# Kernel tuning notes

Hardware: AMD Instinct MI355X
Metric: run time of the kernel (lower is better)

## Reference

```python
import jax, jax.numpy as jnp
import numpy as np

KH, KW = 3, 3
PAD = (1, 1, 1, 1)  # torch F.pad order: (W_left, W_right, H_top, H_bottom)
STRIDE = 1
B, CIN, COUT, H, W = 4, 32, 32, 128, 128


def setup_inputs() -> dict:
    key = jax.random.key(0)
    k1, k2, k3, k4 = jax.random.split(key, 4)
    f = jax.random.normal(k1, (B, CIN, H, W), jnp.float32)
    # orientation field components (cos/sin of a random angle field)
    theta = jax.random.uniform(k2, (B, CIN, H, W), jnp.float32, 0.0, 2.0 * np.pi)
    r0 = jnp.cos(theta)
    r1 = jnp.sin(theta)
    # learned conv weight (nn.Conv2d default uniform init, no bias)
    fan_in = CIN * KH * KW
    bound = 1.0 / np.sqrt(fan_in)
    w = jax.random.uniform(k3, (COUT, CIN, KH, KW), jnp.float32, -bound, bound)
    # frozen wr: (randn * pi * 100) / a with a = 100  ->  randn * pi
    wr = jax.random.normal(k4, (COUT, CIN, KH, KW), jnp.float32) * np.pi
    return {"f": f, "r0": r0, "r1": r1, "w": w, "wr": wr}


def _rot90(w):
    # torch: w.permute(0,1,2,4,3).flip([4]) on the (kh,kw) dims
    return jnp.flip(jnp.swapaxes(w, -1, -2), -1)


def _conv_single(f, r0, r1, w, wr):
    # f, r0, r1: (B, Cin, Hp, Wp);  w, wr: (Cout, Cin, KH, KW)
    Hp, Wp = f.shape[2], f.shape[3]
    he = Hp - PAD[0] - PAD[1]
    we = Wp - PAD[2] - PAD[3]
    s = STRIDE
    out = None
    for i in range(KH):
        for j in range(KW):
            fw = f[:, :, i:i + he:s, j:j + we:s]    # (B, Cin, h, w)
            r0w = r0[:, :, i:i + he:s, j:j + we:s]
            r1w = r1[:, :, i:i + he:s, j:j + we:s]
            c = jnp.cos(wr[:, :, i, j])[None, :, :, None, None]   # (1, Cout, Cin, 1, 1)
            sn = jnp.sin(wr[:, :, i, j])[None, :, :, None, None]
            # lambda_theta: relu of orientation-projected field, (B, Cout, Cin, h, w)
            lam = jax.nn.relu(c * r0w[:, None] + sn * r1w[:, None])
            term = jnp.einsum('bchw,oc,bochw->bohw', fw, w[:, :, i, j], lam)
            out = term if out is None else out + term
    return out  # (B, Cout, h, w)


def _forward(f, r0, r1, w, wr):
    pl, pr, pt, pb = PAD
    pad = ((0, 0), (0, 0), (pt, pb), (pl, pr))
    fp = jnp.pad(f, pad)
    r0p = jnp.pad(r0, pad)
    r1p = jnp.pad(r1, pad)
    orient = jnp.arange(4, dtype=f.dtype) * jnp.asarray(np.pi / 2, f.dtype)
    outs = []
    wk = w
    for o in range(4):
        if o > 0:
            wk = _rot90(wk)
        outs.append(_conv_single(fp, r0p, r1p, wk, wr + orient[o]))
    stacked = jnp.stack(outs, axis=2)              # (B, Cout, 4, h, w)
    idx = jnp.argmax(stacked, axis=2)              # (B, Cout, h, w)
    out = jnp.take_along_axis(stacked, idx[:, :, None], axis=2)[:, :, 0]
    out_r = orient[idx]                            # winning orientation angle
    return out, jnp.cos(out_r), jnp.sin(out_r)


def reference(f, r0, r1, w, wr):
    return _forward(f, r0, r1, w, wr)
```

## Files before the change

kernel.cpp:

```cpp
#include <hip/hip_runtime.h>


typedef float v2f __attribute__((ext_vector_type(2)));

#define B_    4
#define CIN_  32
#define COUT_ 32
#define H_    128
#define W_    128
#define OUTSZ_ (B_ * COUT_ * H_ * W_)

#define TAB_FLOATS (CIN_ * 4 * 9 * 4 * 12)

__global__ __launch_bounds__(256)
void build_wtab(const float* __restrict__ w, const float* __restrict__ wr,
                float* __restrict__ tab)
{
    int idx = blockIdx.x * 256 + threadIdx.x;
    if (idx >= CIN_ * 4 * 9 * 4 * 2) return;
    int k    = idx & 1;
    int r    = idx >> 1;
    int pair = r & 3;
    int r2   = r >> 2;
    int tap  = r2 % 9;
    int t2   = r2 / 9;
    int ocg  = t2 & 3;
    int c    = t2 >> 2;
    int oc   = ocg * 8 + pair * 2 + k;
    int i = tap / 3, j = tap - i * 3;
    int base = (oc * CIN_ + c) * 9;
    float w0 = w[base + i * 3 + j];
    float w1 = w[base + (2 - j) * 3 + i];
    float w2 = w[base + (2 - i) * 3 + (2 - j)];
    float w3 = w[base + j * 3 + (2 - i)];
    float S, C;
    sincosf(wr[base + i * 3 + j], &S, &C);
    float* dst = tab + ((size_t)t2 * 9 + tap) * 48 + pair * 12;
    dst[0 + k]  = C;  dst[2 + k]  = S;
    dst[4 + k]  = w0; dst[6 + k]  = w1;
    dst[8 + k]  = w2; dst[10 + k] = w3;
}

__global__ __launch_bounds__(256, 4)
void orient_conv_kernel(const float* __restrict__ f,
                        const float* __restrict__ r0,
                        const float* __restrict__ r1,
                        const float* __restrict__ tab,
                        float* __restrict__ out)
{
    __shared__ float sIn[3][3][68];

    const int tid   = threadIdx.x;
    const int lane  = tid & 63;
    const int ocg   = __builtin_amdgcn_readfirstlane(tid >> 6);
    const int bid   = blockIdx.x;
    const int b     = bid >> 8;
    const int rem   = bid & 255;
    const int h     = rem >> 1;
    const int wbase = (rem & 1) << 6;

    v2f acc[4][4];
#pragma unroll
    for (int p = 0; p < 4; ++p)
#pragma unroll
        for (int o = 0; o < 4; ++o) acc[p][o] = (v2f)(0.0f);

    for (int c = 0; c < CIN_; ++c) {
        if (tid < 198) {
            int row = tid / 66;
            int col = tid - row * 66;
            int gh = h + row - 1;
            int gw = wbase + col - 1;
            bool ok = ((unsigned)gh < (unsigned)H_) & ((unsigned)gw < (unsigned)W_);
            int off = ((b * CIN_ + c) * H_ + gh) * W_ + gw;
            sIn[0][row][col] = ok ? f[off]  : 0.0f;
            sIn[1][row][col] = ok ? r0[off] : 0.0f;
            sIn[2][row][col] = ok ? r1[off] : 0.0f;
        }
        __syncthreads();

        const float* wt = tab + ((size_t)(c * 4 + ocg) * 9) * 48;

#pragma unroll
        for (int tap = 0; tap < 9; ++tap) {
            const int i = tap / 3;
            const int j = tap - i * 3;
            const int col = lane + j;
            float fv  = sIn[0][i][col];
            float r0s = sIn[1][i][col];
            float r1s = sIn[2][i][col];
            v2f fd;  fd[0]  = fv;  fd[1]  = fv;
            v2f r0d; r0d[0] = r0s; r0d[1] = r0s;
            v2f r1d; r1d[0] = r1s; r1d[1] = r1s;
            const float* wp = wt + tap * 48;
#pragma unroll
            for (int p = 0; p < 4; ++p) {
                const v2f* q = reinterpret_cast<const v2f*>(wp + p * 12);
                v2f Cv = q[0], Sv = q[1];
                v2f w0 = q[2], w1 = q[3], w2 = q[4], w3 = q[5];
                v2f u  = __builtin_elementwise_fma(Cv, r0d, Sv * r1d);
                v2f vv = __builtin_elementwise_fma(Cv, r1d, -(Sv * r0d));
                v2f g0 = __builtin_elementwise_max(u,  (v2f)(0.0f));
                v2f g1 = __builtin_elementwise_max(vv, (v2f)(0.0f));
                v2f g2 = g0 - u;
                v2f g3 = g1 - vv;
                acc[p][0] = __builtin_elementwise_fma(fd * g0, w0, acc[p][0]);
                acc[p][1] = __builtin_elementwise_fma(fd * g1, w1, acc[p][1]);
                acc[p][2] = __builtin_elementwise_fma(fd * g2, w2, acc[p][2]);
                acc[p][3] = __builtin_elementwise_fma(fd * g3, w3, acc[p][3]);
            }
        }
        __syncthreads();
    }

    const float cosv[4] = {1.0f, -4.37113883e-08f, -1.0f, 1.19248806e-08f};
    const float sinv[4] = {0.0f, 1.0f, -8.74227766e-08f, -1.0f};
    const int wcol = wbase + lane;
#pragma unroll
    for (int p = 0; p < 4; ++p) {
#pragma unroll
        for (int k = 0; k < 2; ++k) {
            int oc = ocg * 8 + p * 2 + k;
            float a0 = acc[p][0][k], a1 = acc[p][1][k];
            float a2 = acc[p][2][k], a3 = acc[p][3][k];
            float best = a0; int bi = 0;
            if (a1 > best) { best = a1; bi = 1; }
            if (a2 > best) { best = a2; bi = 2; }
            if (a3 > best) { best = a3; bi = 3; }
            size_t o = ((size_t)(b * COUT_ + oc) * H_ + h) * W_ + wcol;
            out[o]              = best;
            out[o + OUTSZ_]     = cosv[bi];
            out[o + 2 * OUTSZ_] = sinv[bi];
        }
    }
}

extern "C" void kernel_launch(void* const* d_in, const int* in_sizes, int n_in,
                              void* d_out, int out_size, void* d_ws, size_t ws_size,
                              hipStream_t stream)
{
    const float* f  = (const float*)d_in[0];
    const float* r0 = (const float*)d_in[1];
    const float* r1 = (const float*)d_in[2];
    const float* w  = (const float*)d_in[3];
    const float* wr = (const float*)d_in[4];
    float* out = (float*)d_out;
    float* tab = (float*)d_ws;

    build_wtab<<<dim3(36), dim3(256), 0, stream>>>(w, wr, tab);
    orient_conv_kernel<<<dim3(B_ * H_ * 2), dim3(256), 0, stream>>>(
        f, r0, r1, tab, out);
}
```

Measured before the change: 320.2 us.

## Remap threads to output-channel lanes with paired-pixel vectors and interleaved smem tile

Threads now map one-to-one to output channels (32 per wavefront half) and each handles 4 pixels, packed as pairs that sit 32 columns apart, where before each thread handled 8 channels for a single pixel. Blocks grow to 512 threads, and the shared tile is stored interleaved so each thread reads its neighbourhood with float4 LDS loads. The weight table is rearranged to one 8-float record per (cin, tap, oc), read per lane as a vector. The aim is to cut the work of broadcasting scalar weights and to reuse each pixel load across taps, at the cost of per-lane global weight loads and different register pressure.

```diff
diff --git a/kernel.cpp b/kernel.cpp
--- a/kernel.cpp
+++ b/kernel.cpp
@@ -10,104 +10,122 @@
 #define W_    128
 #define OUTSZ_ (B_ * COUT_ * H_ * W_)
 
-#define TAB_FLOATS (CIN_ * 4 * 9 * 4 * 12)
-
 __global__ __launch_bounds__(256)
 void build_wtab(const float* __restrict__ w, const float* __restrict__ wr,
                 float* __restrict__ tab)
 {
     int idx = blockIdx.x * 256 + threadIdx.x;
-    if (idx >= CIN_ * 4 * 9 * 4 * 2) return;
-    int k    = idx & 1;
-    int r    = idx >> 1;
-    int pair = r & 3;
-    int r2   = r >> 2;
-    int tap  = r2 % 9;
-    int t2   = r2 / 9;
-    int ocg  = t2 & 3;
-    int c    = t2 >> 2;
-    int oc   = ocg * 8 + pair * 2 + k;
+    if (idx >= CIN_ * 9 * COUT_) return;
+    int oc  = idx & 31;
+    int t2  = idx >> 5;
+    int tap = t2 % 9;
+    int cc  = t2 / 9;
     int i = tap / 3, j = tap - i * 3;
-    int base = (oc * CIN_ + c) * 9;
+    int base = (oc * CIN_ + cc) * 9;
     float w0 = w[base + i * 3 + j];
     float w1 = w[base + (2 - j) * 3 + i];
     float w2 = w[base + (2 - i) * 3 + (2 - j)];
     float w3 = w[base + j * 3 + (2 - i)];
     float S, C;
     sincosf(wr[base + i * 3 + j], &S, &C);
-    float* dst = tab + ((size_t)t2 * 9 + tap) * 48 + pair * 12;
-    dst[0 + k]  = C;  dst[2 + k]  = S;
-    dst[4 + k]  = w0; dst[6 + k]  = w1;
-    dst[8 + k]  = w2; dst[10 + k] = w3;
+    float* dst = tab + (size_t)idx * 8;
+    dst[0] = C;  dst[1] = S;
+    dst[2] = w0; dst[3] = w1;
+    dst[4] = w2; dst[5] = w3;
+    dst[6] = 0.0f; dst[7] = 0.0f;
 }
 
-__global__ __launch_bounds__(256, 4)
+__global__ __launch_bounds__(512, 4)
 void orient_conv_kernel(const float* __restrict__ f,
                         const float* __restrict__ r0,
                         const float* __restrict__ r1,
                         const float* __restrict__ tab,
                         float* __restrict__ out)
 {
-    __shared__ float sIn[3][3][68];
+    __shared__ float sF[612], sR0[612], sR1[612];
 
     const int tid   = threadIdx.x;
-    const int lane  = tid & 63;
-    const int ocg   = __builtin_amdgcn_readfirstlane(tid >> 6);
+    const int oc    = tid & 31;
+    const int pxg   = tid >> 5;
+    const int p     = pxg << 1;
     const int bid   = blockIdx.x;
     const int b     = bid >> 8;
     const int rem   = bid & 255;
     const int h     = rem >> 1;
     const int wbase = (rem & 1) << 6;
 
-    v2f acc[4][4];
+    int  r_0 = tid / 68, rm0 = tid - r_0 * 68;
+    int  c_0 = rm0 >> 1, s_0 = rm0 & 1;
+    int  gh0 = h + r_0 - 1, gw0 = wbase + c_0 + (s_0 << 5) - 1;
+    bool ok0 = ((unsigned)gh0 < (unsigned)H_) & ((unsigned)gw0 < (unsigned)W_);
+    int  go0 = ok0 ? (gh0 * W_ + gw0) : 0;
+
+    int  sl1 = tid + 512;
+    bool hv1 = sl1 < 612;
+    int  r_1 = sl1 / 68, rm1 = sl1 - r_1 * 68;
+    int  c_1 = rm1 >> 1, s_1 = rm1 & 1;
+    int  gh1 = h + r_1 - 1, gw1 = wbase + c_1 + (s_1 << 5) - 1;
+    bool ok1 = hv1 & ((unsigned)gh1 < (unsigned)H_) & ((unsigned)gw1 < (unsigned)W_);
+    int  go1 = ok1 ? (gh1 * W_ + gw1) : 0;
+
+    const int chanBase = b * (CIN_ * H_ * W_);
+
+    v2f acc[2][4];
 #pragma unroll
-    for (int p = 0; p < 4; ++p)
+    for (int q = 0; q < 2; ++q)
 #pragma unroll
-        for (int o = 0; o < 4; ++o) acc[p][o] = (v2f)(0.0f);
+        for (int o = 0; o < 4; ++o) acc[q][o] = (v2f)(0.0f);
 
-    for (int c = 0; c < CIN_; ++c) {
-        if (tid < 198) {
-            int row = tid / 66;
-            int col = tid - row * 66;
-            int gh = h + row - 1;
-            int gw = wbase + col - 1;
-            bool ok = ((unsigned)gh < (unsigned)H_) & ((unsigned)gw < (unsigned)W_);
-            int off = ((b * CIN_ + c) * H_ + gh) * W_ + gw;
-            sIn[0][row][col] = ok ? f[off]  : 0.0f;
-            sIn[1][row][col] = ok ? r0[off] : 0.0f;
-            sIn[2][row][col] = ok ? r1[off] : 0.0f;
+    for (int cc = 0; cc < CIN_; ++cc) {
+        const int base = chanBase + cc * (H_ * W_);
+        sF [tid] = ok0 ? f [base + go0] : 0.0f;
+        sR0[tid] = ok0 ? r0[base + go0] : 0.0f;
+        sR1[tid] = ok0 ? r1[base + go0] : 0.0f;
+        if (hv1) {
+            sF [sl1] = ok1 ? f [base + go1] : 0.0f;
+            sR0[sl1] = ok1 ? r0[base + go1] : 0.0f;
+            sR1[sl1] = ok1 ? r1[base + go1] : 0.0f;
         }
         __syncthreads();
 
-        const float* wt = tab + ((size_t)(c * 4 + ocg) * 9) * 48;
+        const float* wcc = tab + (((size_t)cc * 9) << 5) * 8 + oc * 8;
 
 #pragma unroll
-        for (int tap = 0; tap < 9; ++tap) {
-            const int i = tap / 3;
-            const int j = tap - i * 3;
-            const int col = lane + j;
-            float fv  = sIn[0][i][col];
-            float r0s = sIn[1][i][col];
-            float r1s = sIn[2][i][col];
-            v2f fd;  fd[0]  = fv;  fd[1]  = fv;
-            v2f r0d; r0d[0] = r0s; r0d[1] = r0s;
-            v2f r1d; r1d[0] = r1s; r1d[1] = r1s;
-            const float* wp = wt + tap * 48;
+        for (int i = 0; i < 3; ++i) {
+            const int wi = i * 68 + (p << 1);
+            float4 fA  = *reinterpret_cast<const float4*>(&sF [wi]);
+            float4 fB  = *reinterpret_cast<const float4*>(&sF [wi + 4]);
+            float4 aA  = *reinterpret_cast<const float4*>(&sR0[wi]);
+            float4 aB  = *reinterpret_cast<const float4*>(&sR0[wi + 4]);
+            float4 bA  = *reinterpret_cast<const float4*>(&sR1[wi]);
+            float4 bB  = *reinterpret_cast<const float4*>(&sR1[wi + 4]);
+            v2f fP[4]  = {{fA.x, fA.y}, {fA.z, fA.w}, {fB.x, fB.y}, {fB.z, fB.w}};
+            v2f r0P[4] = {{aA.x, aA.y}, {aA.z, aA.w}, {aB.x, aB.y}, {aB.z, aB.w}};
+            v2f r1P[4] = {{bA.x, bA.y}, {bA.z, bA.w}, {bB.x, bB.y}, {bB.z, bB.w}};
 #pragma unroll
-            for (int p = 0; p < 4; ++p) {
-                const v2f* q = reinterpret_cast<const v2f*>(wp + p * 12);
-                v2f Cv = q[0], Sv = q[1];
-                v2f w0 = q[2], w1 = q[3], w2 = q[4], w3 = q[5];
-                v2f u  = __builtin_elementwise_fma(Cv, r0d, Sv * r1d);
-                v2f vv = __builtin_elementwise_fma(Cv, r1d, -(Sv * r0d));
-                v2f g0 = __builtin_elementwise_max(u,  (v2f)(0.0f));
-                v2f g1 = __builtin_elementwise_max(vv, (v2f)(0.0f));
-                v2f g2 = g0 - u;
-                v2f g3 = g1 - vv;
-                acc[p][0] = __builtin_elementwise_fma(fd * g0, w0, acc[p][0]);
-                acc[p][1] = __builtin_elementwise_fma(fd * g1, w1, acc[p][1]);
-                acc[p][2] = __builtin_elementwise_fma(fd * g2, w2, acc[p][2]);
-                acc[p][3] = __builtin_elementwise_fma(fd * g3, w3, acc[p][3]);
+            for (int j = 0; j < 3; ++j) {
+                const float* wp = wcc + (i * 3 + j) * 256;
+                float4 wA = *reinterpret_cast<const float4*>(wp);
+                v2f    wB = *reinterpret_cast<const v2f*>(wp + 4);
+                v2f Cd  = {wA.x, wA.x}, Sd  = {wA.y, wA.y};
+                v2f w0d = {wA.z, wA.z}, w1d = {wA.w, wA.w};
+                v2f w2d = {wB.x, wB.x}, w3d = {wB.y, wB.y};
+#pragma unroll
+                for (int q = 0; q < 2; ++q) {
+                    v2f fv  = fP [q + j];
+                    v2f r0v = r0P[q + j];
+                    v2f r1v = r1P[q + j];
+                    v2f u  = __builtin_elementwise_fma(Cd, r0v, Sd * r1v);
+                    v2f vv = __builtin_elementwise_fma(Cd, r1v, -(Sd * r0v));
+                    v2f g0 = __builtin_elementwise_max(u,  (v2f)(0.0f));
+                    v2f g1 = __builtin_elementwise_max(vv, (v2f)(0.0f));
+                    v2f g2 = g0 - u;
+                    v2f g3 = g1 - vv;
+                    acc[q][0] = __builtin_elementwise_fma(fv * g0, w0d, acc[q][0]);
+                    acc[q][1] = __builtin_elementwise_fma(fv * g1, w1d, acc[q][1]);
+                    acc[q][2] = __builtin_elementwise_fma(fv * g2, w2d, acc[q][2]);
+                    acc[q][3] = __builtin_elementwise_fma(fv * g3, w3d, acc[q][3]);
+                }
             }
         }
         __syncthreads();
@@ -115,14 +133,13 @@
 
     const float cosv[4] = {1.0f, -4.37113883e-08f, -1.0f, 1.19248806e-08f};
     const float sinv[4] = {0.0f, 1.0f, -8.74227766e-08f, -1.0f};
-    const int wcol = wbase + lane;
 #pragma unroll
-    for (int p = 0; p < 4; ++p) {
+    for (int q = 0; q < 2; ++q) {
 #pragma unroll
         for (int k = 0; k < 2; ++k) {
-            int oc = ocg * 8 + p * 2 + k;
-            float a0 = acc[p][0][k], a1 = acc[p][1][k];
-            float a2 = acc[p][2][k], a3 = acc[p][3][k];
+            int wcol = wbase + p + q + (k << 5);
+            float a0 = acc[q][0][k], a1 = acc[q][1][k];
+            float a2 = acc[q][2][k], a3 = acc[q][3][k];
             float best = a0; int bi = 0;
             if (a1 > best) { best = a1; bi = 1; }
             if (a2 > best) { best = a2; bi = 2; }
@@ -148,6 +165,6 @@
     float* tab = (float*)d_ws;
 
     build_wtab<<<dim3(36), dim3(256), 0, stream>>>(w, wr, tab);
-    orient_conv_kernel<<<dim3(B_ * H_ * 2), dim3(256), 0, stream>>>(
+    orient_conv_kernel<<<dim3(B_ * H_ * 2), dim3(512), 0, stream>>>(
         f, r0, r1, tab, out);
 }
```

Result: faster. 306.1 us (-4.4%).
